# Performance work log

Measured on AMD Instinct MI355X. Metric: run time of the kernel, lower is better.

## Reference

```python
import jax, jax.numpy as jnp
import numpy as np

B, L, A, D, H = 4, 1024, 8, 1024, 16
DK = D // H


def setup_inputs() -> dict:
    key = jax.random.key(0)
    ks = jax.random.split(key, 11)
    s = 1.0 / np.sqrt(D)
    return {
        "query": jax.random.normal(ks[0], (B, L, A, D), jnp.float32),
        "key": jax.random.normal(ks[1], (B, L, A, D), jnp.float32),
        "value": jax.random.normal(ks[2], (B, L, A, D), jnp.float32),
        "Wq": jax.random.uniform(ks[3], (D, D), jnp.float32, -s, s),
        "bq": jax.random.uniform(ks[4], (D,), jnp.float32, -s, s),
        "Wk": jax.random.uniform(ks[5], (D, D), jnp.float32, -s, s),
        "bk": jax.random.uniform(ks[6], (D,), jnp.float32, -s, s),
        "Wv": jax.random.uniform(ks[7], (D, D), jnp.float32, -s, s),
        "bv": jax.random.uniform(ks[8], (D,), jnp.float32, -s, s),
        "Wo": jax.random.uniform(ks[9], (D, D), jnp.float32, -s, s),
        "bo": jax.random.uniform(ks[10], (D,), jnp.float32, -s, s),
        "d_atrbt": A,
    }


def _proj_heads(x, W, b, a):
    # torch nn.Linear: x @ W.T + b; then view [B, L, a, H, DK] and transpose(2,3)
    y = jnp.einsum("blad,ed->blae", x, W) + b
    nb, nl = y.shape[0], y.shape[1]
    return y.reshape(nb, nl, a, H, DK).transpose(0, 1, 3, 2, 4)  # [B, L, H, a, DK]


def reference(query, key, value, Wq, bq, Wk, bk, Wv, bv, Wo, bo, d_atrbt):
    a = d_atrbt
    q = _proj_heads(query, Wq, bq, a)
    k = _proj_heads(key, Wk, bk, a)
    v = _proj_heads(value, Wv, bv, a)
    # scaled dot-product attention over the attribute axis (size a) per token
    scores = jnp.einsum("blhad,blhed->blhae", q, k) / jnp.sqrt(jnp.asarray(DK, q.dtype))
    p = jax.nn.softmax(scores, axis=-1)  # [B, L, H, a, a]
    x = jnp.einsum("blhae,blhed->blhad", p, v)  # [B, L, H, a, DK]
    nb, nl = x.shape[0], x.shape[1]
    x = x.transpose(0, 1, 3, 2, 4).reshape(nb, nl, a, H * DK)  # [B, L, a, D]
    return jnp.einsum("blad,ed->blae", x, Wo) + bo
```

## Files before the change

### kernel.cpp

```cpp
#include <hip/hip_runtime.h>
#include <hip/hip_bf16.h>
#include <stdint.h>

typedef unsigned short u16;
typedef __bf16 bf16x8 __attribute__((ext_vector_type(8)));
typedef float f32x4 __attribute__((ext_vector_type(4)));

#define MROWS 32768
#define NDIM  1024
#define KDIM  1024
#define NKT   16
#define MHALF 16777216

__device__ __forceinline__ void gload_lds16(const void* g, void* l) {
  __builtin_amdgcn_global_load_lds(
      (__attribute__((address_space(1))) const void*)g,
      (__attribute__((address_space(3))) void*)l,
      16, 0, 0);
}

struct CvtArgs { const float* s[4]; u16* d[4]; };

__global__ __launch_bounds__(256) void cvt4_kernel(CvtArgs ca) {
  const int which = blockIdx.x >> 9;
  const float* s = ca.s[which];
  u16* d = ca.d[which];
  const int i = ((((int)blockIdx.x & 511) * 256) + (int)threadIdx.x) * 8;
  const float4 f0 = *(const float4*)(s + i);
  const float4 f1 = *(const float4*)(s + i + 4);
  bf16x8 h;
  h[0] = (__bf16)f0.x; h[1] = (__bf16)f0.y; h[2] = (__bf16)f0.z; h[3] = (__bf16)f0.w;
  h[4] = (__bf16)f1.x; h[5] = (__bf16)f1.y; h[6] = (__bf16)f1.z; h[7] = (__bf16)f1.w;
  *(bf16x8*)((void*)(d + i)) = h;
}

__global__ __launch_bounds__(256) void cvt_kernel(const float* __restrict__ s,
                                                  u16* __restrict__ d) {
  const int i = ((int)blockIdx.x * 256 + (int)threadIdx.x) * 8;
  const float4 f0 = *(const float4*)(s + i);
  const float4 f1 = *(const float4*)(s + i + 4);
  bf16x8 h;
  h[0] = (__bf16)f0.x; h[1] = (__bf16)f0.y; h[2] = (__bf16)f0.z; h[3] = (__bf16)f0.w;
  h[4] = (__bf16)f1.x; h[5] = (__bf16)f1.y; h[6] = (__bf16)f1.z; h[7] = (__bf16)f1.w;
  *(bf16x8*)((void*)(d + i)) = h;
}

#define SBAR0() __builtin_amdgcn_sched_barrier(0)
#define PH_SYNC() do { SBAR0(); __builtin_amdgcn_s_barrier(); \
    asm volatile("s_waitcnt lgkmcnt(0)" ::: "memory"); SBAR0(); } while (0)
#define PH_END() do { SBAR0(); __builtin_amdgcn_s_barrier(); } while (0)
#define VM4() asm volatile("s_waitcnt vmcnt(4)" ::: "memory")

template <bool OUT_F32>
__global__ __launch_bounds__(512, 2) void gemm8p(const u16* __restrict__ Ab,
                                                 const u16* __restrict__ Bw,
                                                 const float* __restrict__ bias,
                                                 void* __restrict__ Cv,
                                                 int byPerXcd) {
  __shared__ __align__(16) unsigned char As[2][2][16384];
  __shared__ __align__(16) unsigned char Bs[2][2][16384];

  const int bid = (int)blockIdx.x;
  const int xcd = bid & 7;
  const int within = bid >> 3;
  const int by = xcd * byPerXcd + (within >> 2);
  const int bx = within & 3;

  const int t = (int)threadIdx.x;
  const int lane = t & 63;
  const int wid = t >> 6;
  const int wm = wid >> 2;
  const int wn = wid & 3;
  const int bh = wn >> 1;
  const int fr = lane & 15;
  const int hi = lane >> 4;

  size_t gOff[2]; int lOff[2];
#pragma unroll
  for (int i = 0; i < 2; ++i) {
    const int idx = i * 512 + t;
    const int r = idx >> 3, ch = idx & 7;
    gOff[i] = (size_t)r * KDIM + (size_t)((ch ^ (r & 7)) << 3);
    lOff[i] = (i * 512 + (t & ~63)) * 16;
  }
  const u16* Abase = Ab + (size_t)(by * 256) * KDIM;
  const u16* Bbase = Bw + (size_t)(bx * 256) * KDIM;

  auto SA = [&](int tile, int d, int h) {
    const u16* s = Abase + (size_t)(h * 128) * KDIM + tile * 64;
#pragma unroll
    for (int i = 0; i < 2; ++i) gload_lds16(s + gOff[i], &As[d][h][lOff[i]]);
  };
  auto SB = [&](int tile, int d, int h) {
    const u16* s = Bbase + (size_t)(h * 128) * KDIM + tile * 64;
#pragma unroll
    for (int i = 0; i < 2; ++i) gload_lds16(s + gOff[i], &Bs[d][h][lOff[i]]);
  };

  int aOff[8][2], bOff[4][2];
#pragma unroll
  for (int m = 0; m < 8; ++m)
#pragma unroll
    for (int ks = 0; ks < 2; ++ks)
      aOff[m][ks] = (m * 16 + fr) * 128 + (((ks * 4 + hi) ^ (fr & 7)) << 4);
#pragma unroll
  for (int n = 0; n < 4; ++n)
#pragma unroll
    for (int ks = 0; ks < 2; ++ks)
      bOff[n][ks] = ((wn & 1) * 64 + n * 16 + fr) * 128 + (((ks * 4 + hi) ^ (fr & 7)) << 4);

  f32x4 acc[8][4] = {};
  bf16x8 a[4], b[8];

  const unsigned char* Am0 = &As[0][wm][0];
  const unsigned char* Am1 = &As[1][wm][0];
  const unsigned char* Bm0 = &Bs[0][bh][0];
  const unsigned char* Bm1 = &Bs[1][bh][0];

  auto LDA4_0 = [&](int mlo, int ks) {
#pragma unroll
    for (int i = 0; i < 4; ++i)
      a[i] = *(const bf16x8*)((const void*)(Am0 + aOff[mlo + i][ks]));
  };
  auto LDA4_1 = [&](int mlo, int ks) {
#pragma unroll
    for (int i = 0; i < 4; ++i)
      a[i] = *(const bf16x8*)((const void*)(Am1 + aOff[mlo + i][ks]));
  };
  auto LDB8_0 = [&]() {
#pragma unroll
    for (int ks = 0; ks < 2; ++ks)
#pragma unroll
      for (int n = 0; n < 4; ++n)
        b[ks * 4 + n] = *(const bf16x8*)((const void*)(Bm0 + bOff[n][ks]));
  };
  auto LDB8_1 = [&]() {
#pragma unroll
    for (int ks = 0; ks < 2; ++ks)
#pragma unroll
      for (int n = 0; n < 4; ++n)
        b[ks * 4 + n] = *(const bf16x8*)((const void*)(Bm1 + bOff[n][ks]));
  };
  auto MM = [&](int mlo, int bo) {
    __builtin_amdgcn_s_setprio(1);
#pragma unroll
    for (int m = 0; m < 4; ++m)
#pragma unroll
      for (int n = 0; n < 4; ++n)
        acc[mlo + m][n] = __builtin_amdgcn_mfma_f32_16x16x32_bf16(
            a[m], b[bo + n], acc[mlo + m][n], 0, 0, 0);
    __builtin_amdgcn_s_setprio(0);
  };

  SB(0, 0, 0); SB(0, 0, 1); SA(0, 0, 0); SA(0, 0, 1);
  SB(1, 1, 0); SB(1, 1, 1);
  VM4(); SBAR0();
  __builtin_amdgcn_s_barrier();

  for (int j = 0; j < NKT / 2; ++j) {
    const int T1 = 2 * j + 1;
    const int T2 = (2 * j + 2 < NKT) ? 2 * j + 2 : NKT - 1;
    const int T3 = (2 * j + 3 < NKT) ? 2 * j + 3 : NKT - 1;

    LDB8_0(); LDA4_0(0, 0);
    SA(T1, 1, 0);
    PH_SYNC(); MM(0, 0); PH_END();

    LDA4_0(4, 0);
    SA(T1, 1, 1);
    PH_SYNC(); MM(4, 0); PH_END();

    LDA4_0(0, 1);
    SB(T2, 0, 0);
    PH_SYNC(); MM(0, 4); PH_END();

    LDA4_0(4, 1);
    SB(T2, 0, 1);
    PH_SYNC(); MM(4, 4);
    VM4(); PH_END();

    LDB8_1(); LDA4_1(0, 0);
    SA(T2, 0, 0);
    PH_SYNC(); MM(0, 0); PH_END();

    LDA4_1(4, 0);
    SA(T2, 0, 1);
    PH_SYNC(); MM(4, 0); PH_END();

    LDA4_1(0, 1);
    SB(T3, 1, 0);
    PH_SYNC(); MM(0, 4); PH_END();

    LDA4_1(4, 1);
    SB(T3, 1, 1);
    PH_SYNC(); MM(4, 4);
    VM4(); PH_END();
  }
  asm volatile("s_waitcnt vmcnt(0)" ::: "memory");

  const int row0 = by * 256 + wm * 128 + hi * 4;
  const int col0 = bx * 256 + wn * 64 + fr;
#pragma unroll
  for (int n = 0; n < 4; ++n) {
    const int gc = col0 + n * 16;
    const float bv = bias[gc];
#pragma unroll
    for (int m = 0; m < 8; ++m) {
#pragma unroll
      for (int jj = 0; jj < 4; ++jj) {
        const size_t idx = (size_t)(row0 + m * 16 + jj) * NDIM + (size_t)gc;
        const float val = acc[m][n][jj] + bv;
        if constexpr (OUT_F32)
          ((float*)Cv)[idx] = val;
        else
          ((u16*)Cv)[idx] = __builtin_bit_cast(u16, (__bf16)val);
      }
    }
  }
}

__global__ __launch_bounds__(256) void attn_kernel(u16* __restrict__ qx,
                                                   const u16* __restrict__ kb,
                                                   const u16* __restrict__ vb) {
  __shared__ __align__(16) u16 qs[4][8][64];
  __shared__ __align__(16) u16 ks[4][8][64];
  __shared__ __align__(16) u16 vs[4][8][64];
  const int t = threadIdx.x;
  const int lane = t & 63;
  const int w = t >> 6;
  const int unit = blockIdx.x * 4 + w;
  const int bl = unit >> 4;
  const int h = unit & 15;
  const int row = lane >> 3;
  const int c8 = (lane & 7) * 8;
  const size_t goff = (size_t)bl * 8 * 1024 + (size_t)h * 64 + (size_t)row * 1024 + c8;

  *(int4*)((void*)&qs[w][row][c8]) = *(const int4*)((const void*)&qx[goff]);
  *(int4*)((void*)&ks[w][row][c8]) = *(const int4*)((const void*)&kb[goff]);
  *(int4*)((void*)&vs[w][row][c8]) = *(const int4*)((const void*)&vb[goff]);
  __syncthreads();

  const int a = row;
  const int e = lane & 7;
  float s = 0.f;
#pragma unroll
  for (int d8 = 0; d8 < 64; d8 += 8) {
    const bf16x8 qv = *(const bf16x8*)((const void*)&qs[w][a][d8]);
    const bf16x8 kv = *(const bf16x8*)((const void*)&ks[w][e][d8]);
#pragma unroll
    for (int j = 0; j < 8; ++j) s += (float)qv[j] * (float)kv[j];
  }
  s *= 0.125f;

  float mx = s;
#pragma unroll
  for (int o = 1; o < 8; o <<= 1) mx = fmaxf(mx, __shfl_xor(mx, o));
  float p = __expf(s - mx);
  float sum = p;
#pragma unroll
  for (int o = 1; o < 8; o <<= 1) sum += __shfl_xor(sum, o);
  p /= sum;

  float xo[8] = {};
#pragma unroll
  for (int e2 = 0; e2 < 8; ++e2) {
    const float pe = __shfl(p, (lane & 56) + e2);
    const bf16x8 vv = *(const bf16x8*)((const void*)&vs[w][e2][c8]);
#pragma unroll
    for (int j = 0; j < 8; ++j) xo[j] += pe * (float)vv[j];
  }
  bf16x8 hx;
#pragma unroll
  for (int j = 0; j < 8; ++j) hx[j] = (__bf16)xo[j];
  *(int4*)((void*)&qx[goff]) = __builtin_bit_cast(int4, hx);
}

extern "C" void kernel_launch(void* const* d_in, const int* in_sizes, int n_in,
                              void* d_out, int out_size, void* d_ws, size_t ws_size,
                              hipStream_t stream) {
  const float* query = (const float*)d_in[0];
  const float* key   = (const float*)d_in[1];
  const float* value = (const float*)d_in[2];
  const float* Wq = (const float*)d_in[3];
  const float* bq = (const float*)d_in[4];
  const float* Wk = (const float*)d_in[5];
  const float* bk = (const float*)d_in[6];
  const float* Wv = (const float*)d_in[7];
  const float* bv = (const float*)d_in[8];
  const float* Wo = (const float*)d_in[9];
  const float* bo = (const float*)d_in[10];
  (void)in_sizes; (void)n_in; (void)out_size; (void)ws_size;

  const size_t mn = (size_t)MROWS * (size_t)NDIM;

  u16* kb = (u16*)d_out;
  u16* vb = kb + mn;
  u16* qb = (u16*)d_ws;
  u16* Wqb = qb + mn;
  u16* Wkb = Wqb + 1048576;
  u16* Wvb = Wkb + 1048576;
  u16* Wob = Wvb + 1048576;
  u16* Abf = Wob + 1048576;

  CvtArgs ca;
  ca.s[0] = Wq; ca.s[1] = Wk; ca.s[2] = Wv; ca.s[3] = Wo;
  ca.d[0] = Wqb; ca.d[1] = Wkb; ca.d[2] = Wvb; ca.d[3] = Wob;
  cvt4_kernel<<<2048, 256, 0, stream>>>(ca);

  cvt_kernel<<<16384, 256, 0, stream>>>(key, qb);
  gemm8p<false><<<512, 512, 0, stream>>>(qb, Wkb, bk, (void*)kb, 16);
  cvt_kernel<<<16384, 256, 0, stream>>>(value, qb);
  gemm8p<false><<<512, 512, 0, stream>>>(qb, Wvb, bv, (void*)vb, 16);
  cvt_kernel<<<8192, 256, 0, stream>>>(query, Abf);
  gemm8p<false><<<256, 512, 0, stream>>>(Abf, Wqb, bq, (void*)qb, 8);
  cvt_kernel<<<8192, 256, 0, stream>>>(query + MHALF, Abf);
  gemm8p<false><<<256, 512, 0, stream>>>(Abf, Wqb, bq, (void*)(qb + MHALF), 8);

  attn_kernel<<<16384, 256, 0, stream>>>(qb, kb, vb);

  gemm8p<true><<<512, 512, 0, stream>>>(qb, Wob, bo, d_out, 16);
}
```

Before: 468.5 us.

## Fuse next input fp32-to-bf16 conversion into preceding projection GEMM

Folds the standalone fp32→bf16 conversion passes for value and query into the projection GEMMs: each GEMM loads a slice of the next input during its K loop and writes the bf16 copy at the end of each iteration. The key conversion is merged with the weight conversion into one launch. The value and query projections are split into half-size GEMMs so buffers can be ping-ponged through qb, Abf and qb_hi. This removes several kernel launches and lets conversion memory traffic overlap with MFMA compute, at the cost of extra registers and memory pressure inside the GEMM loop.

Result: faster. 455.9 us (-2.7%).

```diff
diff --git a/kernel.cpp b/kernel.cpp
--- a/kernel.cpp
+++ b/kernel.cpp
@@ -21,11 +21,20 @@
 
 struct CvtArgs { const float* s[4]; u16* d[4]; };
 
-__global__ __launch_bounds__(256) void cvt4_kernel(CvtArgs ca) {
-  const int which = blockIdx.x >> 9;
-  const float* s = ca.s[which];
-  u16* d = ca.d[which];
-  const int i = ((((int)blockIdx.x & 511) * 256) + (int)threadIdx.x) * 8;
+__global__ __launch_bounds__(256) void cvt_kw_kernel(const float* __restrict__ key,
+                                                     u16* __restrict__ dkey,
+                                                     CvtArgs ca) {
+  const int bid = (int)blockIdx.x;
+  const float* s; u16* d; int i;
+  if (bid < 16384) {
+    s = key; d = dkey;
+    i = (bid * 256 + (int)threadIdx.x) * 8;
+  } else {
+    const int b2 = bid - 16384;
+    const int which = b2 >> 9;
+    s = ca.s[which]; d = ca.d[which];
+    i = ((b2 & 511) * 256 + (int)threadIdx.x) * 8;
+  }
   const float4 f0 = *(const float4*)(s + i);
   const float4 f1 = *(const float4*)(s + i + 4);
   bf16x8 h;
@@ -34,29 +43,20 @@
   *(bf16x8*)((void*)(d + i)) = h;
 }
 
-__global__ __launch_bounds__(256) void cvt_kernel(const float* __restrict__ s,
-                                                  u16* __restrict__ d) {
-  const int i = ((int)blockIdx.x * 256 + (int)threadIdx.x) * 8;
-  const float4 f0 = *(const float4*)(s + i);
-  const float4 f1 = *(const float4*)(s + i + 4);
-  bf16x8 h;
-  h[0] = (__bf16)f0.x; h[1] = (__bf16)f0.y; h[2] = (__bf16)f0.z; h[3] = (__bf16)f0.w;
-  h[4] = (__bf16)f1.x; h[5] = (__bf16)f1.y; h[6] = (__bf16)f1.z; h[7] = (__bf16)f1.w;
-  *(bf16x8*)((void*)(d + i)) = h;
-}
-
 #define SBAR0() __builtin_amdgcn_sched_barrier(0)
 #define PH_SYNC() do { SBAR0(); __builtin_amdgcn_s_barrier(); \
     asm volatile("s_waitcnt lgkmcnt(0)" ::: "memory"); SBAR0(); } while (0)
 #define PH_END() do { SBAR0(); __builtin_amdgcn_s_barrier(); } while (0)
 #define VM4() asm volatile("s_waitcnt vmcnt(4)" ::: "memory")
 
-template <bool OUT_F32>
+template <bool OUT_F32, int CVTP>
 __global__ __launch_bounds__(512, 2) void gemm8p(const u16* __restrict__ Ab,
                                                  const u16* __restrict__ Bw,
                                                  const float* __restrict__ bias,
                                                  void* __restrict__ Cv,
-                                                 int byPerXcd) {
+                                                 int byPerXcd,
+                                                 const float* __restrict__ cvt_src,
+                                                 u16* __restrict__ cvt_dst) {
   __shared__ __align__(16) unsigned char As[2][2][16384];
   __shared__ __align__(16) unsigned char Bs[2][2][16384];
 
@@ -152,6 +152,8 @@
     __builtin_amdgcn_s_setprio(0);
   };
 
+  const int ngrid = (int)gridDim.x;
+
   SB(0, 0, 0); SB(0, 0, 1); SA(0, 0, 0); SA(0, 0, 1);
   SB(1, 1, 0); SB(1, 1, 1);
   VM4(); SBAR0();
@@ -162,6 +164,16 @@
     const int T2 = (2 * j + 2 < NKT) ? 2 * j + 2 : NKT - 1;
     const int T3 = (2 * j + 3 < NKT) ? 2 * j + 3 : NKT - 1;
 
+    float4 cf[CVTP ? CVTP : 1][2];
+    if constexpr (CVTP > 0) {
+#pragma unroll
+      for (int p = 0; p < CVTP; ++p) {
+        const size_t b8i = ((size_t)(j * CVTP + p) * ngrid + bid) * 512 + t;
+        cf[p][0] = ((const float4*)cvt_src)[b8i * 2];
+        cf[p][1] = ((const float4*)cvt_src)[b8i * 2 + 1];
+      }
+    }
+
     LDB8_0(); LDA4_0(0, 0);
     SA(T1, 1, 0);
     PH_SYNC(); MM(0, 0); PH_END();
@@ -194,7 +206,21 @@
     LDA4_1(4, 1);
     SB(T3, 1, 1);
     PH_SYNC(); MM(4, 4);
-    VM4(); PH_END();
+    VM4();
+
+    if constexpr (CVTP > 0) {
+#pragma unroll
+      for (int p = 0; p < CVTP; ++p) {
+        const size_t b8i = ((size_t)(j * CVTP + p) * ngrid + bid) * 512 + t;
+        bf16x8 h;
+        h[0] = (__bf16)cf[p][0].x; h[1] = (__bf16)cf[p][0].y;
+        h[2] = (__bf16)cf[p][0].z; h[3] = (__bf16)cf[p][0].w;
+        h[4] = (__bf16)cf[p][1].x; h[5] = (__bf16)cf[p][1].y;
+        h[6] = (__bf16)cf[p][1].z; h[7] = (__bf16)cf[p][1].w;
+        *(bf16x8*)((void*)(cvt_dst + b8i * 8)) = h;
+      }
+    }
+    PH_END();
   }
   asm volatile("s_waitcnt vmcnt(0)" ::: "memory");
 
@@ -301,22 +327,26 @@
   u16* Wvb = Wkb + 1048576;
   u16* Wob = Wvb + 1048576;
   u16* Abf = Wob + 1048576;
+  u16* qb_hi = qb + MHALF;
 
   CvtArgs ca;
   ca.s[0] = Wq; ca.s[1] = Wk; ca.s[2] = Wv; ca.s[3] = Wo;
   ca.d[0] = Wqb; ca.d[1] = Wkb; ca.d[2] = Wvb; ca.d[3] = Wob;
-  cvt4_kernel<<<2048, 256, 0, stream>>>(ca);
-
-  cvt_kernel<<<16384, 256, 0, stream>>>(key, qb);
-  gemm8p<false><<<512, 512, 0, stream>>>(qb, Wkb, bk, (void*)kb, 16);
-  cvt_kernel<<<16384, 256, 0, stream>>>(value, qb);
-  gemm8p<false><<<512, 512, 0, stream>>>(qb, Wvb, bv, (void*)vb, 16);
-  cvt_kernel<<<8192, 256, 0, stream>>>(query, Abf);
-  gemm8p<false><<<256, 512, 0, stream>>>(Abf, Wqb, bq, (void*)qb, 8);
-  cvt_kernel<<<8192, 256, 0, stream>>>(query + MHALF, Abf);
-  gemm8p<false><<<256, 512, 0, stream>>>(Abf, Wqb, bq, (void*)(qb + MHALF), 8);
+  cvt_kw_kernel<<<18432, 256, 0, stream>>>(key, qb, ca);
+
+  gemm8p<false, 1><<<512, 512, 0, stream>>>(qb, Wkb, bk, (void*)kb, 16,
+                                            value, Abf);
+  gemm8p<false, 2><<<256, 512, 0, stream>>>(Abf, Wvb, bv, (void*)vb, 8,
+                                            value + MHALF, qb);
+  gemm8p<false, 2><<<256, 512, 0, stream>>>(qb, Wvb, bv, (void*)(vb + MHALF), 8,
+                                            query, qb_hi);
+  gemm8p<false, 2><<<256, 512, 0, stream>>>(qb_hi, Wqb, bq, (void*)qb, 8,
+                                            query + MHALF, Abf);
+  gemm8p<false, 0><<<256, 512, 0, stream>>>(Abf, Wqb, bq, (void*)qb_hi, 8,
+                                            nullptr, nullptr);
 
   attn_kernel<<<16384, 256, 0, stream>>>(qb, kb, vb);
 
-  gemm8p<true><<<512, 512, 0, stream>>>(qb, Wob, bo, d_out, 16);
-}
+  gemm8p<true, 0><<<512, 512, 0, stream>>>(qb, Wob, bo, d_out, 16,
+                                           nullptr, nullptr);
+}
```

## Fuse fp32-to-bf16 activation conversion into projection GEMM loads

Applied to the files above, without the earlier changes.

Adds a GEMM kernel that loads fp32 activation tiles directly into LDS and converts them to bf16 in registers before the MFMAs. This drops the separate conversion kernels and the bf16 staging buffer for the Q/K/V projections, removing a full extra write and read of each activation tensor. In exchange, A tiles take twice the LDS space and global bandwidth per tile, conversion work moves into the inner loop, and the pipeline uses a simpler two-stage buffer with a barrier every iteration.

Result: slower. 512.4 us (+9.4%).

```diff
diff --git a/kernel.cpp b/kernel.cpp
--- a/kernel.cpp
+++ b/kernel.cpp
@@ -9,8 +9,6 @@
 #define MROWS 32768
 #define NDIM  1024
 #define KDIM  1024
-#define NKT   16
-#define MHALF 16777216
 
 __device__ __forceinline__ void gload_lds16(const void* g, void* l) {
   __builtin_amdgcn_global_load_lds(
@@ -34,28 +32,143 @@
   *(bf16x8*)((void*)(d + i)) = h;
 }
 
-__global__ __launch_bounds__(256) void cvt_kernel(const float* __restrict__ s,
-                                                  u16* __restrict__ d) {
-  const int i = ((int)blockIdx.x * 256 + (int)threadIdx.x) * 8;
-  const float4 f0 = *(const float4*)(s + i);
-  const float4 f1 = *(const float4*)(s + i + 4);
-  bf16x8 h;
-  h[0] = (__bf16)f0.x; h[1] = (__bf16)f0.y; h[2] = (__bf16)f0.z; h[3] = (__bf16)f0.w;
-  h[4] = (__bf16)f1.x; h[5] = (__bf16)f1.y; h[6] = (__bf16)f1.z; h[7] = (__bf16)f1.w;
-  *(bf16x8*)((void*)(d + i)) = h;
-}
-
 #define SBAR0() __builtin_amdgcn_sched_barrier(0)
+#define VM6() asm volatile("s_waitcnt vmcnt(6)" ::: "memory")
+
+__global__ __launch_bounds__(512, 2) void gemm8f(const float* __restrict__ Af,
+                                                 const u16* __restrict__ Bw,
+                                                 const float* __restrict__ bias,
+                                                 u16* __restrict__ Cv,
+                                                 int byPerXcd) {
+  __shared__ __align__(16) unsigned char As[2][32768];
+  __shared__ __align__(16) unsigned char Bs[2][16384];
+
+  const int bid = (int)blockIdx.x;
+  const int xcd = bid & 7;
+  const int within = bid >> 3;
+  const int by = xcd * byPerXcd + (within >> 2);
+  const int bx = within & 3;
+
+  const int t = (int)threadIdx.x;
+  const int lane = t & 63;
+  const int wid = t >> 6;
+  const int wm = wid >> 2;
+  const int wn = wid & 3;
+  const int fr = lane & 15;
+  const int hi = lane >> 4;
+
+  size_t aG[4]; int aL[4];
+#pragma unroll
+  for (int i = 0; i < 4; ++i) {
+    const int idx = i * 512 + t;
+    const int r = idx >> 3, ch = idx & 7;
+    aG[i] = (size_t)r * KDIM + (size_t)((ch ^ (r & 7)) << 2);
+    aL[i] = (i * 512 + (t & ~63)) * 16;
+  }
+  size_t bG[2]; int bL[2];
+#pragma unroll
+  for (int i = 0; i < 2; ++i) {
+    const int idx = i * 512 + t;
+    const int r = idx >> 2, ch = idx & 3;
+    bG[i] = (size_t)r * KDIM + (size_t)((ch ^ (r & 3)) << 3);
+    bL[i] = (i * 512 + (t & ~63)) * 16;
+  }
+  const float* Abase = Af + (size_t)(by * 256) * KDIM;
+  const u16* Bbase = Bw + (size_t)(bx * 256) * KDIM;
+
+  auto SA = [&](int tile, int d) {
+    const float* s = Abase + tile * 32;
+#pragma unroll
+    for (int i = 0; i < 4; ++i) gload_lds16(s + aG[i], &As[d][aL[i]]);
+  };
+  auto SB = [&](int tile, int d) {
+    const u16* s = Bbase + tile * 32;
+#pragma unroll
+    for (int i = 0; i < 2; ++i) gload_lds16(s + bG[i], &Bs[d][bL[i]]);
+  };
+
+  int aOffF[8][2];
+#pragma unroll
+  for (int m = 0; m < 8; ++m)
+#pragma unroll
+    for (int c = 0; c < 2; ++c)
+      aOffF[m][c] = (wm * 128 + m * 16 + fr) * 128 + (((hi * 2 + c) ^ (fr & 7)) << 4);
+  int bOffF[4];
+#pragma unroll
+  for (int n = 0; n < 4; ++n)
+    bOffF[n] = (wn * 64 + n * 16 + fr) * 64 + ((hi ^ (fr & 3)) << 4);
+
+  f32x4 acc[8][4] = {};
+
+  SA(0, 0); SB(0, 0); SA(1, 1); SB(1, 1);
+  VM6(); SBAR0();
+  __builtin_amdgcn_s_barrier();
+
+  for (int kt = 0; kt < 32; ++kt) {
+    const int d = kt & 1;
+
+    bf16x8 a8[8], b4[4];
+#pragma unroll
+    for (int m = 0; m < 8; ++m) {
+      const f32x4 x0 = *(const f32x4*)((const void*)(As[d] + aOffF[m][0]));
+      const f32x4 x1 = *(const f32x4*)((const void*)(As[d] + aOffF[m][1]));
+      bf16x8 h;
+      h[0] = (__bf16)x0[0]; h[1] = (__bf16)x0[1]; h[2] = (__bf16)x0[2]; h[3] = (__bf16)x0[3];
+      h[4] = (__bf16)x1[0]; h[5] = (__bf16)x1[1]; h[6] = (__bf16)x1[2]; h[7] = (__bf16)x1[3];
+      a8[m] = h;
+    }
+#pragma unroll
+    for (int n = 0; n < 4; ++n)
+      b4[n] = *(const bf16x8*)((const void*)(Bs[d] + bOffF[n]));
+
+    asm volatile("s_waitcnt lgkmcnt(0)" ::: "memory");
+    SBAR0();
+    __builtin_amdgcn_s_barrier();
+    SBAR0();
+
+    const int tn = (kt + 2 < 32) ? kt + 2 : 31;
+    SA(tn, d); SB(tn, d);
+
+    __builtin_amdgcn_s_setprio(1);
+#pragma unroll
+    for (int m = 0; m < 8; ++m)
+#pragma unroll
+      for (int n = 0; n < 4; ++n)
+        acc[m][n] = __builtin_amdgcn_mfma_f32_16x16x32_bf16(a8[m], b4[n], acc[m][n], 0, 0, 0);
+    __builtin_amdgcn_s_setprio(0);
+
+    VM6();
+    SBAR0();
+    __builtin_amdgcn_s_barrier();
+  }
+
+  const int row0 = by * 256 + wm * 128 + hi * 4;
+  const int col0 = bx * 256 + wn * 64 + fr;
+#pragma unroll
+  for (int n = 0; n < 4; ++n) {
+    const int gc = col0 + n * 16;
+    const float bv = bias[gc];
+#pragma unroll
+    for (int m = 0; m < 8; ++m) {
+#pragma unroll
+      for (int jj = 0; jj < 4; ++jj) {
+        const size_t idx = (size_t)(row0 + m * 16 + jj) * NDIM + (size_t)gc;
+        Cv[idx] = __builtin_bit_cast(u16, (__bf16)(acc[m][n][jj] + bv));
+      }
+    }
+  }
+}
+
 #define PH_SYNC() do { SBAR0(); __builtin_amdgcn_s_barrier(); \
     asm volatile("s_waitcnt lgkmcnt(0)" ::: "memory"); SBAR0(); } while (0)
 #define PH_END() do { SBAR0(); __builtin_amdgcn_s_barrier(); } while (0)
 #define VM4() asm volatile("s_waitcnt vmcnt(4)" ::: "memory")
-
-template <bool OUT_F32>
+#define NKT 16
+
 __global__ __launch_bounds__(512, 2) void gemm8p(const u16* __restrict__ Ab,
                                                  const u16* __restrict__ Bw,
                                                  const float* __restrict__ bias,
-                                                 void* __restrict__ Cv,
+                                                 float* __restrict__ Cv,
                                                  int byPerXcd) {
   __shared__ __align__(16) unsigned char As[2][2][16384];
   __shared__ __align__(16) unsigned char Bs[2][2][16384];
@@ -209,11 +322,7 @@
 #pragma unroll
       for (int jj = 0; jj < 4; ++jj) {
         const size_t idx = (size_t)(row0 + m * 16 + jj) * NDIM + (size_t)gc;
-        const float val = acc[m][n][jj] + bv;
-        if constexpr (OUT_F32)
-          ((float*)Cv)[idx] = val;
-        else
-          ((u16*)Cv)[idx] = __builtin_bit_cast(u16, (__bf16)val);
+        Cv[idx] = acc[m][n][jj] + bv;
       }
     }
   }
@@ -300,23 +409,17 @@
   u16* Wkb = Wqb + 1048576;
   u16* Wvb = Wkb + 1048576;
   u16* Wob = Wvb + 1048576;
-  u16* Abf = Wob + 1048576;
 
   CvtArgs ca;
   ca.s[0] = Wq; ca.s[1] = Wk; ca.s[2] = Wv; ca.s[3] = Wo;
   ca.d[0] = Wqb; ca.d[1] = Wkb; ca.d[2] = Wvb; ca.d[3] = Wob;
   cvt4_kernel<<<2048, 256, 0, stream>>>(ca);
 
-  cvt_kernel<<<16384, 256, 0, stream>>>(key, qb);
-  gemm8p<false><<<512, 512, 0, stream>>>(qb, Wkb, bk, (void*)kb, 16);
-  cvt_kernel<<<16384, 256, 0, stream>>>(value, qb);
-  gemm8p<false><<<512, 512, 0, stream>>>(qb, Wvb, bv, (void*)vb, 16);
-  cvt_kernel<<<8192, 256, 0, stream>>>(query, Abf);
-  gemm8p<false><<<256, 512, 0, stream>>>(Abf, Wqb, bq, (void*)qb, 8);
-  cvt_kernel<<<8192, 256, 0, stream>>>(query + MHALF, Abf);
-  gemm8p<false><<<256, 512, 0, stream>>>(Abf, Wqb, bq, (void*)(qb + MHALF), 8);
+  gemm8f<<<512, 512, 0, stream>>>(key,   Wkb, bk, kb, 16);
+  gemm8f<<<512, 512, 0, stream>>>(value, Wvb, bv, vb, 16);
+  gemm8f<<<512, 512, 0, stream>>>(query, Wqb, bq, qb, 16);
 
   attn_kernel<<<16384, 256, 0, stream>>>(qb, kb, vb);
 
-  gemm8p<true><<<512, 512, 0, stream>>>(qb, Wob, bo, d_out, 16);
-}
+  gemm8p<<<512, 512, 0, stream>>>(qb, Wob, bo, (float*)d_out, 16);
+}
```
